# Performance work log

Measured on AMD Instinct MI355X. Metric: run time of the kernel, lower is better.

## Reference

```python
import jax, jax.numpy as jnp
import numpy as np

IOU_THRESHOLDS = (0.5, 0.75)
B, N, G = 256, 4000, 50


def _iou(amin, amax, bmin, bmax):
    # broadcasted temporal IoU: anchors [N,1] vs boxes [1,G] -> [N,G]
    inter = jnp.maximum(jnp.minimum(amax, bmax) - jnp.maximum(amin, bmin), 0.0)
    union = (amax - amin) + (bmax - bmin) - inter
    return inter / union


def _greedy_tp(segments, gts, thr):
    # segments: [N,2], gts: [G,2]. Replicates AP.get_values greedy matching:
    # for each label (in order), claim the first (lowest-index) unused proposal
    # whose IoU > thr. Final used-mask == is_TP.
    ious = _iou(segments[:, 0:1], segments[:, 1:2], gts[None, :, 0], gts[None, :, 1])  # [N,G]
    pot = ious > thr
    n = segments.shape[0]

    def step(used, col):  # col: [N] bool, candidates for this label
        cand = col & ~used
        idx = jnp.argmax(cand)  # first True (argmax of bool is first max)
        used = jnp.where(jnp.any(cand), used.at[idx].set(True), used)
        return used, None

    used, _ = jax.lax.scan(step, jnp.zeros((n,), jnp.bool_), pot.T)
    return used  # [N] bool


def _ap_for_threshold(scores, segments, labels, thr):
    is_tp = jax.vmap(lambda s, g: _greedy_tp(s, g, thr))(segments, labels)  # [B,N]
    conf = scores.reshape(-1)                       # [B*N]
    tp = is_tp.reshape(-1).astype(jnp.float32)
    order = jnp.argsort(-conf)                      # sort by confidence, descending
    tp = tp[order]
    n_labels = labels.shape[0] * labels.shape[1]
    m = tp.shape[0]
    acc_tp = jnp.cumsum(tp)
    precision = acc_tp / (jnp.arange(m, dtype=jnp.float32) + 1.0)
    recall = acc_tp / jnp.float32(n_labels)
    # curve = [[1,0]] then (recall, precision) reversed; AP = sum(|dx| * cummax(y)[:-1])
    x = jnp.concatenate([jnp.ones((1,), jnp.float32), recall[::-1]])
    y = jnp.concatenate([jnp.zeros((1,), jnp.float32), precision[::-1]])
    y_max = jax.lax.cummax(y, axis=0)
    x_diff = jnp.abs(jnp.diff(x))
    return jnp.sum(x_diff * y_max[:-1])


def setup_inputs() -> dict:
    key = jax.random.key(0)
    k1, k2, k3, k4, k5 = jax.random.split(key, 5)
    scores = jax.random.uniform(k1, (B, N), dtype=jnp.float32)
    p_start = jax.random.uniform(k2, (B, N), dtype=jnp.float32) * 0.9
    p_len = jax.random.uniform(k3, (B, N), dtype=jnp.float32) * 0.1 + 0.005
    segments = jnp.stack([p_start, p_start + p_len], axis=-1)  # [B,N,2], start<end
    g_start = jax.random.uniform(k4, (B, G), dtype=jnp.float32) * 0.9
    g_len = jax.random.uniform(k5, (B, G), dtype=jnp.float32) * 0.1 + 0.005
    labels = jnp.stack([g_start, g_start + g_len], axis=-1)    # [B,G,2]
    return {"scores": scores, "segments": segments, "labels": labels}


def reference(scores, segments, labels):
    # returns AP at each IoU threshold, shape [len(IOU_THRESHOLDS)]
    return jnp.stack([_ap_for_threshold(scores, segments, labels, t) for t in IOU_THRESHOLDS])
```

## Files before the change

### kernel.cpp

```cpp
#include <hip/hip_runtime.h>


#define B_ 256
#define N_ 4000
#define G_ 50
#define M_ (B_ * N_)
#define NL_ (B_ * G_)
#define NBKT 2048
#define KP 16
#define TILE (NL_ / KP)

#define M0_ 0x1.000001p-1
#define M1_ 0x1.800001p-1

typedef unsigned long long u64;

__device__ __forceinline__ unsigned bucket_of(float c) {
    unsigned b = (unsigned)(c * 2048.0f);
    return b > (NBKT - 1) ? (NBKT - 1) : b;
}

__global__ __launch_bounds__(1024) void tp_kernel(
    const float* __restrict__ seg,
    const float* __restrict__ gts,
    const float* __restrict__ conf,
    int* __restrict__ tpIdx,
    int* __restrict__ cnt,
    unsigned short* __restrict__ pbh)
{
    const int tid  = threadIdx.x;
    const int lane = tid & 63;
    const int wv   = tid >> 6;
    const int b    = blockIdx.x;

    __shared__ float2 gtl[G_];
    __shared__ u64 cand[2][G_][64];
    __shared__ unsigned hls[NBKT];
    __shared__ int lcnt[2];

    #pragma unroll
    for (int k = 0; k < NBKT / 1024; ++k) hls[k * 1024 + tid] = 0u;
    if (tid < G_) gtl[tid] = ((const float2*)gts)[b * G_ + tid];
    if (tid < 2) lcnt[tid] = 0;
    __syncthreads();

    const float* cb = conf + (size_t)b * N_;
    #pragma unroll
    for (int s = 0; s < 4; ++s) {
        int n = s * 1024 + tid;
        if (n < N_) atomicAdd(&hls[bucket_of(cb[n])], 1u);
    }

    const float2* sb = (const float2*)(seg + (size_t)b * (N_ * 2));
    float pmin[4], pmax[4], plen[4];
    #pragma unroll
    for (int s = 0; s < 4; ++s) {
        int n = s * 1024 + tid;
        if (n < N_) { float2 v = sb[n]; pmin[s] = v.x; pmax[s] = v.y; }
        else { pmin[s] = 1e9f; pmax[s] = 1e9f; }
        plen[s] = pmax[s] - pmin[s];
    }
    for (int g = 0; g < G_; ++g) {
        float2 gt = gtl[g];
        float glen = gt.y - gt.x;
        u64 m0[4], m1[4];
        #pragma unroll
        for (int s = 0; s < 4; ++s) {
            float inter = fmaxf(fminf(pmax[s], gt.y) - fmaxf(pmin[s], gt.x), 0.0f);
            float uni = plen[s] + glen - inter;
            double di = (double)inter;
            double du = (double)uni;
            m0[s] = __ballot(di > M0_ * du);
            m1[s] = __ballot(di > M1_ * du);
        }
        if (lane == 0) {
            #pragma unroll
            for (int s = 0; s < 4; ++s) {
                cand[0][g][s * 16 + wv] = m0[s];
                cand[1][g][s * 16 + wv] = m1[s];
            }
        }
    }
    __syncthreads();

    #pragma unroll
    for (int k = 0; k < NBKT / 1024; ++k) {
        int bin = k * 1024 + tid;
        pbh[(size_t)b * NBKT + bin] = (unsigned short)hls[bin];
    }

    if (wv < 2) {
        const int thr_i = wv;
        u64 used = 0ull;
        for (int g = 0; g < G_; ++g) {
            u64 c = cand[thr_i][g][lane] & ~used;
            u64 ball = __ballot(c != 0ull);
            if (ball) {
                int fl = __ffsll(ball) - 1;
                if (lane == fl) used |= (c & (0ull - c));
            }
        }
        int cpop = __popcll(used);
        if (cpop) {
            int j = atomicAdd(&lcnt[thr_i], cpop);
            u64 u = used;
            while (u) {
                int bit = __ffsll(u) - 1;
                u &= u - 1;
                tpIdx[thr_i * NL_ + b * G_ + j++] = b * N_ + lane * 64 + bit;
            }
        }
    }
    __syncthreads();
    if (tid < 2) cnt[tid * B_ + b] = lcnt[tid];
}

__global__ __launch_bounds__(256) void s1_kernel(
    unsigned short* __restrict__ pbh,
    unsigned* __restrict__ total)
{
    __shared__ unsigned sc[256];
    const int bin = blockIdx.x;
    const int b = threadIdx.x;
    unsigned v = pbh[(size_t)b * NBKT + bin];
    sc[b] = v;
    __syncthreads();
    for (int off = 1; off < 256; off <<= 1) {
        unsigned add = (b >= off) ? sc[b - off] : 0u;
        __syncthreads();
        sc[b] += add;
        __syncthreads();
    }
    pbh[(size_t)b * NBKT + bin] = (unsigned short)(sc[b] - v);
    if (b == 255) total[bin] = sc[255];
}

__global__ __launch_bounds__(1024) void s2_kernel(
    const unsigned* __restrict__ total, unsigned* __restrict__ binStart)
{
    __shared__ unsigned part[1024];
    int t = threadIdx.x;
    uint2 v2 = ((const uint2*)total)[t];
    unsigned s = v2.x + v2.y;
    part[t] = s;
    __syncthreads();
    for (int off = 1; off < 1024; off <<= 1) {
        unsigned add = (t >= off) ? part[t - off] : 0u;
        __syncthreads();
        part[t] += add;
        __syncthreads();
    }
    unsigned base = (t == 0) ? 0u : part[t - 1];
    ((uint2*)binStart)[t] = make_uint2(base, base + v2.x);
}

__global__ __launch_bounds__(1024) void scatter_kernel(
    const float* __restrict__ conf,
    const unsigned short* __restrict__ pbh,
    const unsigned* __restrict__ binStart,
    u64* __restrict__ sKey)
{
    __shared__ unsigned baseB[NBKT];
    __shared__ unsigned lofs[NBKT];
    const int tid = threadIdx.x;
    const int b = blockIdx.x;
    #pragma unroll
    for (int k = 0; k < NBKT / 1024; ++k) {
        int bin = k * 1024 + tid;
        baseB[bin] = binStart[bin] + pbh[(size_t)b * NBKT + bin];
        lofs[bin] = 0u;
    }
    __syncthreads();
    const float* cb = conf + (size_t)b * N_;
    #pragma unroll
    for (int s = 0; s < 4; ++s) {
        int n = s * 1024 + tid;
        if (n < N_) {
            float c = cb[n];
            unsigned bin = bucket_of(c);
            unsigned lo = atomicAdd(&lofs[bin], 1u);
            unsigned idx = (unsigned)(b * N_ + n);
            sKey[baseB[bin] + lo] = ((u64)__float_as_uint(c) << 32) | (u64)(0xFFFFFFFFu - idx);
        }
    }
}

__global__ __launch_bounds__(256) void rank_kernel(
    const float* __restrict__ conf,
    const int* __restrict__ tpIdx,
    const int* __restrict__ cnt,
    const unsigned* __restrict__ total,
    const unsigned* __restrict__ binStart,
    const u64* __restrict__ sKey,
    int* __restrict__ tpRank)
{
    const int lane = threadIdx.x & 63;
    const int w = (blockIdx.x << 2) | (threadIdx.x >> 6);
    if (w >= 2 * NL_) return;
    const int thr_i = w / NL_;
    const int t = w - thr_i * NL_;
    const int batch = t / G_;
    const int j = t - batch * G_;

    if (j < cnt[thr_i * B_ + batch]) {
        int e = tpIdx[thr_i * NL_ + t];
        float c = conf[e];
        u64 keyE = ((u64)__float_as_uint(c) << 32) | (u64)(0xFFFFFFFFu - (unsigned)e);
        unsigned bin = bucket_of(c);
        unsigned lo = binStart[bin], n = total[bin];
        int r = M_ - (int)lo - (int)n;
        for (unsigned base = 0; base < n; base += 64) {
            unsigned k = base + lane;
            bool pred = (k < n) && (sKey[lo + k] > keyE);
            r += (int)__popcll(__ballot(pred));
        }
        if (lane == 0) tpRank[thr_i * NL_ + t] = r;
    } else {
        if (lane == 0) tpRank[thr_i * NL_ + t] = M_ + t;
    }
}

__global__ __launch_bounds__(256) void pos1_kernel(
    const int* __restrict__ tpRank,
    int* __restrict__ pcount)
{
    __shared__ alignas(16) int tile[TILE];
    const int k = blockIdx.y, thr_i = blockIdx.z;
    const int* base = tpRank + thr_i * NL_;
    for (int i = threadIdx.x; i < TILE; i += 256)
        tile[i] = base[k * TILE + i];
    __syncthreads();

    const int t0 = blockIdx.x * 1024 + threadIdx.x;
    int r[4], c[4] = {0, 0, 0, 0};
    #pragma unroll
    for (int j = 0; j < 4; ++j) {
        int t = t0 + j * 256;
        r[j] = (t < NL_) ? base[t] : -1;
    }
    const int4* l4 = (const int4*)tile;
    #pragma unroll 4
    for (int i = 0; i < TILE / 4; ++i) {
        int4 v = l4[i];
        #pragma unroll
        for (int j = 0; j < 4; ++j)
            c[j] += (v.x < r[j]) + (v.y < r[j]) + (v.z < r[j]) + (v.w < r[j]);
    }
    #pragma unroll
    for (int j = 0; j < 4; ++j) {
        int t = t0 + j * 256;
        if (t < NL_) pcount[(thr_i * KP + k) * NL_ + t] = c[j];
    }
}

__global__ __launch_bounds__(1024) void ap_kernel(
    const int* __restrict__ tpRank,
    const int* __restrict__ pcount,
    float* __restrict__ out)
{
    const int C = 13;
    __shared__ int sr[NL_];
    __shared__ float cmax[1024];
    __shared__ double red[1024];
    int thr_i = blockIdx.x;
    int t = threadIdx.x;

    #pragma unroll
    for (int j = 0; j < C; ++j) {
        int tt = t + j * 1024;
        if (tt < NL_) {
            int p = 0;
            #pragma unroll
            for (int k = 0; k < KP; ++k)
                p += pcount[(thr_i * KP + k) * NL_ + tt];
            sr[p] = tpRank[thr_i * NL_ + tt];
        }
    }
    __syncthreads();

    float pr[C]; int rk[C];
    #pragma unroll
    for (int k = 0; k < C; ++k) {
        int i = t * C + k;
        rk[k] = (i < NL_) ? sr[i] : 0x7FFFFFFF;
        pr[k] = (rk[k] < M_) ? (float)(i + 1) / (float)(rk[k] + 1) : -1.0f;
    }
    float suf[C];
    float run = -1.0f;
    #pragma unroll
    for (int k = C - 1; k >= 0; --k) { run = fmaxf(run, pr[k]); suf[k] = run; }

    cmax[t] = run;
    __syncthreads();
    for (int off = 1; off < 1024; off <<= 1) {
        float v = cmax[t];
        float o = (t + off < 1024) ? cmax[t + off] : -1.0f;
        __syncthreads();
        cmax[t] = fmaxf(v, o);
        __syncthreads();
    }
    float follow = (t + 1 < 1024) ? cmax[t + 1] : -1.0f;

    double acc = 0.0;
    #pragma unroll
    for (int k = 0; k < C; ++k) {
        int i = t * C + k;
        if (rk[k] >= 1 && rk[k] < M_) {
            float smax = fmaxf(suf[k], follow);
            float rhi = (float)(i + 1) / 12800.0f;
            float rlo = (float)i / 12800.0f;
            acc += (double)((rhi - rlo) * smax);
        }
    }
    red[t] = acc;
    __syncthreads();
    for (int off = 512; off >= 1; off >>= 1) {
        if (t < off) red[t] += red[t + off];
        __syncthreads();
    }
    if (t == 0) out[thr_i] = (float)red[0];
}

extern "C" void kernel_launch(void* const* d_in, const int* in_sizes, int n_in,
                              void* d_out, int out_size, void* d_ws, size_t ws_size,
                              hipStream_t stream) {
    const float* scores = (const float*)d_in[0];
    const float* seg    = (const float*)d_in[1];
    const float* gts    = (const float*)d_in[2];
    float* out = (float*)d_out;

    char* p = (char*)d_ws;
    int*            cnt        = (int*)p;             p += 4096;
    int*            tpIdx      = (int*)p;             p += 2 * NL_ * 4;
    int*            tpRank     = (int*)p;             p += 2 * NL_ * 4;
    unsigned*       total      = (unsigned*)p;        p += NBKT * 4;
    unsigned*       binStart   = (unsigned*)p;        p += NBKT * 4;
    unsigned short* pbh        = (unsigned short*)p;  p += (size_t)B_ * NBKT * 2;
    u64*            sKey       = (u64*)p;             p += (size_t)M_ * 8;
    int*            pcount     = (int*)sKey;
    (void)ws_size; (void)in_sizes; (void)n_in; (void)out_size;

    tp_kernel<<<B_, 1024, 0, stream>>>(seg, gts, scores, tpIdx, cnt, pbh);
    s1_kernel<<<NBKT, 256, 0, stream>>>(pbh, total);
    s2_kernel<<<1, 1024, 0, stream>>>(total, binStart);
    scatter_kernel<<<B_, 1024, 0, stream>>>(scores, pbh, binStart, sKey);
    rank_kernel<<<(2 * NL_ + 3) / 4, 256, 0, stream>>>(scores, tpIdx, cnt,
                                                       total, binStart, sKey, tpRank);
    pos1_kernel<<<dim3(13, KP, 2), 256, 0, stream>>>(tpRank, pcount);
    ap_kernel<<<2, 1024, 0, stream>>>(tpRank, pcount, out);
}
```

Baseline: 186.6 us.

## Replace quadratic rank-count sort with in-block bucket sort fused into AP kernel

Drops the all-pairs position-count kernel and its global pcount buffer. The AP kernel now sorts TP ranks itself: it builds a shared-memory bucket histogram, prefix-sums it, scatters ranks into buckets, and does a small local count within each bucket to find the final position. This removes one launch and the O(NL^2) comparison work. The cost is that the whole sort now runs in just two blocks, and uneven bucket sizes could lengthen the per-bucket scans.

After: 169.8 us. 9.0% less time.

```diff
diff --git a/kernel.cpp b/kernel.cpp
--- a/kernel.cpp
+++ b/kernel.cpp
@@ -7,8 +7,6 @@
 #define M_ (B_ * N_)
 #define NL_ (B_ * G_)
 #define NBKT 2048
-#define KP 16
-#define TILE (NL_ / KP)
 
 #define M0_ 0x1.000001p-1
 #define M1_ 0x1.800001p-1
@@ -220,62 +218,74 @@
     }
 }
 
-__global__ __launch_bounds__(256) void pos1_kernel(
+__global__ __launch_bounds__(1024) void sortap_kernel(
     const int* __restrict__ tpRank,
-    int* __restrict__ pcount)
-{
-    __shared__ alignas(16) int tile[TILE];
-    const int k = blockIdx.y, thr_i = blockIdx.z;
-    const int* base = tpRank + thr_i * NL_;
-    for (int i = threadIdx.x; i < TILE; i += 256)
-        tile[i] = base[k * TILE + i];
-    __syncthreads();
-
-    const int t0 = blockIdx.x * 1024 + threadIdx.x;
-    int r[4], c[4] = {0, 0, 0, 0};
-    #pragma unroll
-    for (int j = 0; j < 4; ++j) {
-        int t = t0 + j * 256;
-        r[j] = (t < NL_) ? base[t] : -1;
-    }
-    const int4* l4 = (const int4*)tile;
-    #pragma unroll 4
-    for (int i = 0; i < TILE / 4; ++i) {
-        int4 v = l4[i];
-        #pragma unroll
-        for (int j = 0; j < 4; ++j)
-            c[j] += (v.x < r[j]) + (v.y < r[j]) + (v.z < r[j]) + (v.w < r[j]);
-    }
-    #pragma unroll
-    for (int j = 0; j < 4; ++j) {
-        int t = t0 + j * 256;
-        if (t < NL_) pcount[(thr_i * KP + k) * NL_ + t] = c[j];
-    }
-}
-
-__global__ __launch_bounds__(1024) void ap_kernel(
-    const int* __restrict__ tpRank,
-    const int* __restrict__ pcount,
     float* __restrict__ out)
 {
     const int C = 13;
+    union U1 { unsigned part[1024]; float cmax[1024]; };
+    union U2 { unsigned hist[NBKT]; double red[1024]; };
     __shared__ int sr[NL_];
-    __shared__ float cmax[1024];
-    __shared__ double red[1024];
-    int thr_i = blockIdx.x;
-    int t = threadIdx.x;
-
-    #pragma unroll
-    for (int j = 0; j < C; ++j) {
-        int tt = t + j * 1024;
-        if (tt < NL_) {
-            int p = 0;
-            #pragma unroll
-            for (int k = 0; k < KP; ++k)
-                p += pcount[(thr_i * KP + k) * NL_ + tt];
-            sr[p] = tpRank[thr_i * NL_ + tt];
-        }
-    }
+    __shared__ U1 u1;
+    __shared__ U2 u2;
+    const int thr_i = blockIdx.x;
+    const int t = threadIdx.x;
+
+    u2.hist[t] = 0u; u2.hist[t + 1024] = 0u;
+    __syncthreads();
+
+    int r[C]; unsigned beta[C];
+    #pragma unroll
+    for (int k = 0; k < C; ++k) {
+        int i = t + k * 1024;
+        if (i < NL_) {
+            int rr = tpRank[thr_i * NL_ + i];
+            r[k] = rr;
+            unsigned bb = ((unsigned)rr) >> 9;
+            beta[k] = bb > (NBKT - 1) ? (NBKT - 1) : bb;
+            atomicAdd(&u2.hist[beta[k]], 1u);
+        } else { r[k] = 0; beta[k] = 0xFFFFFFFFu; }
+    }
+    __syncthreads();
+
+    unsigned h0 = u2.hist[2 * t], h1 = u2.hist[2 * t + 1];
+    u1.part[t] = h0 + h1;
+    __syncthreads();
+    for (int off = 1; off < 1024; off <<= 1) {
+        unsigned add = (t >= off) ? u1.part[t - off] : 0u;
+        __syncthreads();
+        u1.part[t] += add;
+        __syncthreads();
+    }
+    unsigned base = (t == 0) ? 0u : u1.part[t - 1];
+    __syncthreads();
+    u2.hist[2 * t] = base;
+    u2.hist[2 * t + 1] = base + h0;
+    __syncthreads();
+
+    #pragma unroll
+    for (int k = 0; k < C; ++k)
+        if (beta[k] != 0xFFFFFFFFu) {
+            unsigned slot = atomicAdd(&u2.hist[beta[k]], 1u);
+            sr[slot] = r[k];
+        }
+    __syncthreads();
+
+    int p[C];
+    #pragma unroll
+    for (int k = 0; k < C; ++k) {
+        if (beta[k] != 0xFFFFFFFFu) {
+            unsigned st = (beta[k] == 0u) ? 0u : u2.hist[beta[k] - 1];
+            unsigned en = u2.hist[beta[k]];
+            int c = 0;
+            for (unsigned j = st; j < en; ++j) c += (sr[j] < r[k]);
+            p[k] = (int)st + c;
+        } else p[k] = -1;
+    }
+    __syncthreads();
+    #pragma unroll
+    for (int k = 0; k < C; ++k)
+        if (p[k] >= 0) sr[p[k]] = r[k];
     __syncthreads();
 
     float pr[C]; int rk[C];
@@ -290,16 +300,16 @@
     #pragma unroll
     for (int k = C - 1; k >= 0; --k) { run = fmaxf(run, pr[k]); suf[k] = run; }
 
-    cmax[t] = run;
+    u1.cmax[t] = run;
     __syncthreads();
     for (int off = 1; off < 1024; off <<= 1) {
-        float v = cmax[t];
-        float o = (t + off < 1024) ? cmax[t + off] : -1.0f;
-        __syncthreads();
-        cmax[t] = fmaxf(v, o);
-        __syncthreads();
-    }
-    float follow = (t + 1 < 1024) ? cmax[t + 1] : -1.0f;
+        float v = u1.cmax[t];
+        float o = (t + off < 1024) ? u1.cmax[t + off] : -1.0f;
+        __syncthreads();
+        u1.cmax[t] = fmaxf(v, o);
+        __syncthreads();
+    }
+    float follow = (t + 1 < 1024) ? u1.cmax[t + 1] : -1.0f;
 
     double acc = 0.0;
     #pragma unroll
@@ -312,13 +322,14 @@
             acc += (double)((rhi - rlo) * smax);
         }
     }
-    red[t] = acc;
+    __syncthreads();
+    u2.red[t] = acc;
     __syncthreads();
     for (int off = 512; off >= 1; off >>= 1) {
-        if (t < off) red[t] += red[t + off];
-        __syncthreads();
-    }
-    if (t == 0) out[thr_i] = (float)red[0];
+        if (t < off) u2.red[t] += u2.red[t + off];
+        __syncthreads();
+    }
+    if (t == 0) out[thr_i] = (float)u2.red[0];
 }
 
 extern "C" void kernel_launch(void* const* d_in, const int* in_sizes, int n_in,
@@ -337,7 +348,6 @@
     unsigned*       binStart   = (unsigned*)p;        p += NBKT * 4;
     unsigned short* pbh        = (unsigned short*)p;  p += (size_t)B_ * NBKT * 2;
     u64*            sKey       = (u64*)p;             p += (size_t)M_ * 8;
-    int*            pcount     = (int*)sKey;
     (void)ws_size; (void)in_sizes; (void)n_in; (void)out_size;
 
     tp_kernel<<<B_, 1024, 0, stream>>>(seg, gts, scores, tpIdx, cnt, pbh);
@@ -346,6 +356,5 @@
     scatter_kernel<<<B_, 1024, 0, stream>>>(scores, pbh, binStart, sKey);
     rank_kernel<<<(2 * NL_ + 3) / 4, 256, 0, stream>>>(scores, tpIdx, cnt,
                                                        total, binStart, sKey, tpRank);
-    pos1_kernel<<<dim3(13, KP, 2), 256, 0, stream>>>(tpRank, pcount);
-    ap_kernel<<<2, 1024, 0, stream>>>(tpRank, pcount, out);
-}
+    sortap_kernel<<<2, 1024, 0, stream>>>(tpRank, out);
+}
```
